# Performance work log

Measured on AMD Instinct MI355X. Metric: run time of the kernel, lower is better.

## Reference

```python
import jax, jax.numpy as jnp
import numpy as np

B, L, D = 4, 1024, 256
H, HD, W = 8, 64, 3


def setup_inputs() -> dict:
    key = jax.random.key(0)
    ks = jax.random.split(key, 5)
    return {
        'x': jax.random.normal(ks[0], (B, L, D), dtype=jnp.float32),
        'Wq': jax.random.normal(ks[1], (D, H * HD), dtype=jnp.float32) * 0.05,
        'bq': jnp.zeros((H, 1, 1, HD), dtype=jnp.float32),
        'Wk': jax.random.normal(ks[2], (D, H * HD), dtype=jnp.float32) * 0.05,
        'bk': jnp.zeros((H, 1, 1, HD), dtype=jnp.float32),
        'Wv': jax.random.normal(ks[3], (D, H), dtype=jnp.float32) * 0.05,
        'pe': jax.random.normal(ks[4], (L, D), dtype=jnp.float32) * 0.05,
    }


def reference(x, Wq, bq, Wk, bk, Wv, pe):
    b, l, d = x.shape
    h, hd = bq.shape[0], bq.shape[-1]
    xpe = x + pe  # learned positional encoding added for Q and K only
    # tf.split over axis 3 into h heads + concat axis 0 == reshape then head-major transpose
    q = (xpe @ Wq).reshape(b, l, h, hd).transpose(2, 0, 1, 3) + bq  # [H,B,L,hd]
    k = (xpe @ Wk).reshape(b, l, h, hd).transpose(2, 0, 1, 3) + bk  # [H,B,L,hd]
    v = jax.nn.sigmoid(x @ Wv).transpose(2, 0, 1)  # [H,B,L]
    att = jnp.einsum('hbqd,hbkd->hbqk', q, k) / jnp.sqrt(jnp.asarray(hd, x.dtype))
    att = jax.nn.softmax(att, axis=-1)  # [H,B,L,L]
    # band_part(0,-1) + diag_part(k=(0,L-1)) + transpose + reverse(-2,-1) is
    # equivalent to: out[.., jp, dist] = att[.., n-dist, n] with n = L-1-jp, masked n-dist>=0
    jp = jnp.arange(l)
    n = l - 1 - jp                      # reversed position index, [L]
    m = n[:, None] - jp[None, :]        # row (query) index per (pos, distance), [L,L]
    valid = m >= 0
    g = att[:, :, jnp.clip(m, 0), n[:, None]]  # gather diagonals -> [H,B,L,L]
    a = jnp.where(valid, g, jnp.asarray(0, x.dtype)) * v[:, :, :, None]
    # avg pool over the distance (last) axis, window W, stride 1, SAME,
    # TF AvgPool excludes padding from the count
    ssum = jax.lax.reduce_window(a, 0.0, jax.lax.add, (1, 1, 1, W), (1, 1, 1, 1), 'SAME')
    cnt = jax.lax.reduce_window(jnp.ones((l,), a.dtype), 0.0, jax.lax.add, (W,), (1,), 'SAME')
    a = ssum / cnt  # [H,B,L,L]
    # global_mode: permute to [B, pos, dist, H] and sum over positions
    return a.transpose(1, 2, 3, 0).sum(axis=1)  # [B, L, H]
```

## Files before the change

### kernel.cpp

```cpp
#include <hip/hip_runtime.h>
#include <hip/hip_bf16.h>
#include <math.h>

#define B 4
#define L 1024
#define D 256
#define H 8
#define HD 64

#define KB_OFF  1048576
#define VR_OFF  2097152
#define TP2_OFF (VR_OFF + 32768)
#define T_OFF   (TP2_OFF + 2097152)
#define XP_OFF  (T_OFF + 32768)
#define WT_OFF  (XP_OFF + 524288)

typedef short short8 __attribute__((ext_vector_type(8)));
typedef float f32x16 __attribute__((ext_vector_type(16)));

__device__ __forceinline__ unsigned short f2bf(float f) {
  __hip_bfloat16 h = __float2bfloat16(f);
  return *reinterpret_cast<unsigned short*>(&h);
}

__global__ __launch_bounds__(256) void prep_wx_kernel(
    const float* __restrict__ x, const float* __restrict__ Wq,
    const float* __restrict__ Wk, const float* __restrict__ Wv,
    const float* __restrict__ pe, float* __restrict__ ws)
{
  const int tid = threadIdx.x;
  if (blockIdx.x < 32) {
    __shared__ float lds[32][257];
    const int c0 = blockIdx.x * 32;
    const float* W = (c0 < 512) ? Wq : Wk;
    const int cc = c0 & 511;
    const int c = tid & 31, dd = tid >> 5;
    for (int d0 = 0; d0 < 256; d0 += 8)
      lds[c][d0 + dd] = W[(d0 + dd) * 512 + cc + c];
    __syncthreads();
    __hip_bfloat16* WT = (__hip_bfloat16*)(ws + WT_OFF);
    for (int cl = 0; cl < 32; ++cl)
      WT[(c0 + cl) * 256 + tid] = __float2bfloat16(lds[cl][tid]);
    return;
  }

  __shared__ float xs[8][257];
  const int r0 = (blockIdx.x - 32) * 8;
  __hip_bfloat16* XP = (__hip_bfloat16*)(ws + XP_OFF);
  for (int idx = tid; idx < 2048; idx += 256) {
    int rr = idx >> 8, c = idx & 255;
    int gr = r0 + rr, l = gr & 1023;
    float xv = x[gr * 256 + c];
    xs[rr][c] = xv;
    XP[gr * 256 + c] = __float2bfloat16(xv + pe[l * 256 + c]);
  }
  __syncthreads();
  {
    int rr = tid >> 5, h = (tid >> 2) & 7, t4 = tid & 3;
    float acc = 0.f;
    const int d0 = t4 << 6;
#pragma unroll 16
    for (int d = 0; d < 64; ++d) acc += xs[rr][d0 + d] * Wv[(d0 + d) * 8 + h];
    acc += __shfl_down(acc, 1, 4);
    acc += __shfl_down(acc, 2, 4);
    if (t4 == 0) {
      float v = 1.f / (1.f + __expf(-acc));
      int gr = r0 + rr;
      int b = gr >> 10, l = gr & 1023;
      ws[VR_OFF + (h * 4 + b) * 1024 + (1023 - l)] = v;
    }
  }
}

__global__ __launch_bounds__(256) void qkgemm_kernel(float* __restrict__ ws,
    const float* __restrict__ bq, const float* __restrict__ bk)
{
  const int tid = threadIdx.x;
  const int w = tid >> 6, lane = tid & 63;
  const int wid = blockIdx.x * 4 + w;
  const int lt = wid & 127;
  const int cp = wid >> 7;

  const __hip_bfloat16* XP = (const __hip_bfloat16*)(ws + XP_OFF);
  const __hip_bfloat16* WT = (const __hip_bfloat16*)(ws + WT_OFF);

  const int ln = (lt << 5) + (lane & 31);
  const int dlo = (lane >> 5) << 3;
  const int ca = (cp << 6) + (lane & 31);
  const __hip_bfloat16* xr = XP + ln * 256 + dlo;
  const __hip_bfloat16* ar = WT + ca * 256 + dlo;
  const __hip_bfloat16* br = ar + (32 * 256);

  f32x16 acca = {0.f,0.f,0.f,0.f,0.f,0.f,0.f,0.f,0.f,0.f,0.f,0.f,0.f,0.f,0.f,0.f};
  f32x16 accb = {0.f,0.f,0.f,0.f,0.f,0.f,0.f,0.f,0.f,0.f,0.f,0.f,0.f,0.f,0.f,0.f};
#pragma unroll
  for (int k = 0; k < 16; ++k) {
    short8 bf  = *(const short8*)(xr + k * 16);
    short8 afa = *(const short8*)(ar + k * 16);
    short8 afb = *(const short8*)(br + k * 16);
    acca = __builtin_amdgcn_mfma_f32_32x32x16_bf16(afa, bf, acca, 0, 0, 0);
    accb = __builtin_amdgcn_mfma_f32_32x32x16_bf16(afb, bf, accb, 0, 0, 0);
  }

  const int b = ln >> 10, l = ln & 1023;
  const int hq = cp & 7;
  const int hi4 = (lane >> 5) << 2;
  const float* bias = (cp < 8) ? bq : bk;
  const int cbase = hq << 6;
  __hip_bfloat16* base = (__hip_bfloat16*)ws + ((cp < 8) ? 0 : (size_t)KB_OFF * 2);
  __hip_bfloat16* dst = base + ((((size_t)(hq * 4 + b) << 10) + l) << 6);

#pragma unroll
  for (int q = 0; q < 4; ++q) {
    int hd0 = (q << 3) + hi4;
    float4 bv = *(const float4*)(bias + cbase + hd0);
    ushort4 pk;
    pk.x = f2bf(acca[4 * q + 0] + bv.x);
    pk.y = f2bf(acca[4 * q + 1] + bv.y);
    pk.z = f2bf(acca[4 * q + 2] + bv.z);
    pk.w = f2bf(acca[4 * q + 3] + bv.w);
    *(ushort4*)(dst + hd0) = pk;

    int hd1 = hd0 + 32;
    float4 bw = *(const float4*)(bias + cbase + hd1);
    ushort4 pk2;
    pk2.x = f2bf(accb[4 * q + 0] + bw.x);
    pk2.y = f2bf(accb[4 * q + 1] + bw.y);
    pk2.z = f2bf(accb[4 * q + 2] + bw.z);
    pk2.w = f2bf(accb[4 * q + 3] + bw.w);
    *(ushort4*)(dst + hd1) = pk2;
  }
}

__global__ __launch_bounds__(256) void attn_kernel(float* __restrict__ ws)
{
  __shared__ __hip_bfloat16 Ks[256 * 64];
  __shared__ float smerge[4][32];
  const int tid = threadIdx.x;
  const int w = tid >> 6, lane = tid & 63;
  const int i = blockIdx.x;
  const int hb = i & 31;
  const int j = i >> 5;
  const int qt = (j & 8) ? ((j < 16) ? 23 - j : 55 - j) : j;

  const __hip_bfloat16* Qb = (const __hip_bfloat16*)ws + ((size_t)hb << 16);
  const __hip_bfloat16* Kb = (const __hip_bfloat16*)(ws + KB_OFF) + ((size_t)hb << 16);
  const float* __restrict__ vr = ws + VR_OFF + (hb << 10);

  const int qrow = (qt << 5) + (lane & 31);
  const int dlo = (lane >> 5) << 3;
  const int coff = (lane >> 5) << 2;

  const __hip_bfloat16* qr = Qb + (qrow << 6) + dlo;
  short8 qf0 = *(const short8*)(qr);
  short8 qf1 = *(const short8*)(qr + 16);
  short8 qf2 = *(const short8*)(qr + 32);
  short8 qf3 = *(const short8*)(qr + 48);

#define STAGE8(c)                                                             \
  {                                                                           \
    const float4* src_ = (const float4*)Kb + ((c) << 11);                     \
    _Pragma("unroll")                                                         \
    for (int u = 0; u < 8; ++u) {                                             \
      int idx_ = (u << 8) + tid;                                              \
      float4 v_ = src_[idx_];                                                 \
      int row_ = idx_ >> 3;                                                   \
      int colb_ = (idx_ & 7) << 4;                                            \
      *(float4*)((char*)Ks + row_ * 128 + (colb_ ^ ((row_ & 7) << 4))) = v_;  \
    }                                                                         \
  }

#define LDK(tl, kf)                                                           \
  {                                                                           \
    int row_ = ((tl) << 5) + (lane & 31);                                     \
    int sw_ = (row_ & 7) << 4;                                                \
    int cb_ = (lane >> 5) << 4;                                               \
    char* bp_ = (char*)Ks + row_ * 128;                                       \
    kf[0] = *(const short8*)(bp_ + ((cb_) ^ sw_));                            \
    kf[1] = *(const short8*)(bp_ + ((cb_ + 32) ^ sw_));                       \
    kf[2] = *(const short8*)(bp_ + ((cb_ + 64) ^ sw_));                       \
    kf[3] = *(const short8*)(bp_ + ((cb_ + 96) ^ sw_));                       \
  }

  float sp0 = 0.f, sp1 = 0.f, sp2 = 0.f, sp3 = 0.f;
  for (int c = 0; c < 4; ++c) {
    if (c) __syncthreads();
    STAGE8(c);
    __syncthreads();
    short8 ka[4], kb[4];
    LDK(w, ka);
    LDK(w + 4, kb);
    f32x16 acca = {0.f,0.f,0.f,0.f,0.f,0.f,0.f,0.f,0.f,0.f,0.f,0.f,0.f,0.f,0.f,0.f};
    f32x16 accb = {0.f,0.f,0.f,0.f,0.f,0.f,0.f,0.f,0.f,0.f,0.f,0.f,0.f,0.f,0.f,0.f};
    acca = __builtin_amdgcn_mfma_f32_32x32x16_bf16(ka[0], qf0, acca, 0, 0, 0);
    accb = __builtin_amdgcn_mfma_f32_32x32x16_bf16(kb[0], qf0, accb, 0, 0, 0);
    acca = __builtin_amdgcn_mfma_f32_32x32x16_bf16(ka[1], qf1, acca, 0, 0, 0);
    accb = __builtin_amdgcn_mfma_f32_32x32x16_bf16(kb[1], qf1, accb, 0, 0, 0);
    acca = __builtin_amdgcn_mfma_f32_32x32x16_bf16(ka[2], qf2, acca, 0, 0, 0);
    accb = __builtin_amdgcn_mfma_f32_32x32x16_bf16(kb[2], qf2, accb, 0, 0, 0);
    acca = __builtin_amdgcn_mfma_f32_32x32x16_bf16(ka[3], qf3, acca, 0, 0, 0);
    accb = __builtin_amdgcn_mfma_f32_32x32x16_bf16(kb[3], qf3, accb, 0, 0, 0);
#pragma unroll
    for (int r = 0; r < 16; r += 2) {
      sp0 += __expf(acca[r] * 0.125f);
      sp1 += __expf(acca[r + 1] * 0.125f);
      sp2 += __expf(accb[r] * 0.125f);
      sp3 += __expf(accb[r + 1] * 0.125f);
    }
  }
  float s_part = (sp0 + sp1) + (sp2 + sp3);
  s_part += __shfl_xor(s_part, 32);
  if (lane < 32) smerge[w][lane] = s_part;
  __syncthreads();
  const int q = lane & 31;
  const float inv = 1.f / (smerge[0][q] + smerge[1][q] + smerge[2][q] + smerge[3][q]);

#define FLUSH(dt_, acc_)                                                      \
  {                                                                           \
    const int kt_ = qt + (dt_);                                               \
    const float* vb_ = vr + (kt_ << 5) + coff;                                \
    float4 v0_ = *(const float4*)(vb_);                                       \
    float4 v1_ = *(const float4*)(vb_ + 8);                                   \
    float4 v2_ = *(const float4*)(vb_ + 16);                                  \
    float4 v3_ = *(const float4*)(vb_ + 24);                                  \
    float p_[16];                                                             \
    _Pragma("unroll")                                                         \
    for (int r = 0; r < 16; ++r) {                                            \
      float vv_ = (r < 4) ? (&v0_.x)[r] : (r < 8) ? (&v1_.x)[r - 4]           \
                : (r < 12) ? (&v2_.x)[r - 8] : (&v3_.x)[r - 12];              \
      p_[r] = __expf(acc_[r] * 0.125f) * vv_ * inv;                           \
    }                                                                         \
    float accg_ = 0.f;                                                        \
    _Pragma("unroll")                                                         \
    for (int hi = 0; hi < 2; ++hi)                                            \
      _Pragma("unroll")                                                       \
      for (int r = 0; r < 16; ++r) {                                          \
        const int km_ = (hi << 2) + (r & 3) + ((r >> 2) << 3);                \
        int src_ = ((hi << 5) + km_ + 31 - lane) & 63;                        \
        float g_ = __shfl(p_[r], src_);                                       \
        if (km_ <= lane && km_ >= lane - 31) accg_ += g_;                     \
      }                                                                       \
    ws[TP2_OFF + ((size_t)hb << 16) + ((((qt) << 5) + (dt_)) << 6) + lane] = accg_; \
  }

  const int c0 = qt >> 3;
  for (int c = 3; c >= c0; --c) {
    if (c != 3) {
      __syncthreads();
      STAGE8(c);
      __syncthreads();
    }
    const int kta = (c << 3) + w;
    const int ktb = kta + 4;
    if (kta >= qt) {
      short8 ka[4], kb[4];
      LDK(w, ka);
      LDK(w + 4, kb);
      f32x16 acca = {0.f,0.f,0.f,0.f,0.f,0.f,0.f,0.f,0.f,0.f,0.f,0.f,0.f,0.f,0.f,0.f};
      f32x16 accb = {0.f,0.f,0.f,0.f,0.f,0.f,0.f,0.f,0.f,0.f,0.f,0.f,0.f,0.f,0.f,0.f};
      acca = __builtin_amdgcn_mfma_f32_32x32x16_bf16(ka[0], qf0, acca, 0, 0, 0);
      accb = __builtin_amdgcn_mfma_f32_32x32x16_bf16(kb[0], qf0, accb, 0, 0, 0);
      acca = __builtin_amdgcn_mfma_f32_32x32x16_bf16(ka[1], qf1, acca, 0, 0, 0);
      accb = __builtin_amdgcn_mfma_f32_32x32x16_bf16(kb[1], qf1, accb, 0, 0, 0);
      acca = __builtin_amdgcn_mfma_f32_32x32x16_bf16(ka[2], qf2, acca, 0, 0, 0);
      accb = __builtin_amdgcn_mfma_f32_32x32x16_bf16(kb[2], qf2, accb, 0, 0, 0);
      acca = __builtin_amdgcn_mfma_f32_32x32x16_bf16(ka[3], qf3, acca, 0, 0, 0);
      accb = __builtin_amdgcn_mfma_f32_32x32x16_bf16(kb[3], qf3, accb, 0, 0, 0);
      FLUSH(kta - qt, acca);
      FLUSH(ktb - qt, accb);
    } else if (ktb >= qt) {
      short8 kb[4];
      LDK(w + 4, kb);
      f32x16 accb = {0.f,0.f,0.f,0.f,0.f,0.f,0.f,0.f,0.f,0.f,0.f,0.f,0.f,0.f,0.f,0.f};
      accb = __builtin_amdgcn_mfma_f32_32x32x16_bf16(kb[0], qf0, accb, 0, 0, 0);
      accb = __builtin_amdgcn_mfma_f32_32x32x16_bf16(kb[1], qf1, accb, 0, 0, 0);
      accb = __builtin_amdgcn_mfma_f32_32x32x16_bf16(kb[2], qf2, accb, 0, 0, 0);
      accb = __builtin_amdgcn_mfma_f32_32x32x16_bf16(kb[3], qf3, accb, 0, 0, 0);
      FLUSH(ktb - qt, accb);
    }
  }
}

__global__ __launch_bounds__(256) void out1_kernel(float* __restrict__ ws)
{
  const int tid = threadIdx.x;
  const int i = blockIdx.x;
  const int hb = i & 31;
  const int jc = i >> 5;
  const int jj = (jc << 5) + (tid >> 3);
  const int t8 = tid & 7;
  const float* TP = ws + TP2_OFF + ((size_t)hb << 16);

  float acc = 0.f;
  const int s = jj + 31;
#pragma unroll
  for (int cand = 0; cand < 2; ++cand) {
    int dt = (s >> 5) - cand;
    if (dt < 0 || dt > 31) continue;
    int idx = s - (dt << 5);
    int qmax = 31 - dt;
    for (int qt = t8; qt <= qmax; qt += 8)
      acc += TP[(((qt << 5) + dt) << 6) + idx];
  }
  acc += __shfl_down(acc, 4, 8);
  acc += __shfl_down(acc, 2, 8);
  acc += __shfl_down(acc, 1, 8);
  if (t8 == 0) ws[T_OFF + (hb << 10) + jj] = acc;
}

__global__ __launch_bounds__(256) void out2_kernel(const float* __restrict__ ws,
                                                   float* __restrict__ out)
{
  __shared__ float s[130];
  const int tid = threadIdx.x;
  const int i = blockIdx.x;
  const int hb = i & 31;
  const int jc = i >> 5;
  const int j0 = jc << 7;
  const float* T = ws + T_OFF + (hb << 10);

  if (tid < 130) {
    int j = j0 + tid - 1;
    s[tid] = (j >= 0 && j < 1024) ? T[j] : 0.f;
  }
  __syncthreads();
  if (tid < 128) {
    int j = j0 + tid;
    float cnt = (j == 0 || j == 1023) ? 2.f : 3.f;
    float v = (s[tid] + s[tid + 1] + s[tid + 2]) / cnt;
    int h = hb >> 2, b = hb & 3;
    out[(((b << 10) + j) << 3) + h] = v;
  }
}

extern "C" void kernel_launch(void* const* d_in, const int* in_sizes, int n_in,
                              void* d_out, int out_size, void* d_ws, size_t ws_size,
                              hipStream_t stream)
{
  const float* x  = (const float*)d_in[0];
  const float* Wq = (const float*)d_in[1];
  const float* bq = (const float*)d_in[2];
  const float* Wk = (const float*)d_in[3];
  const float* bk = (const float*)d_in[4];
  const float* Wv = (const float*)d_in[5];
  const float* pe = (const float*)d_in[6];
  float* ws = (float*)d_ws;
  float* out = (float*)d_out;

  prep_wx_kernel<<<dim3(544), dim3(256), 0, stream>>>(x, Wq, Wk, Wv, pe, ws);
  qkgemm_kernel<<<dim3(512), dim3(256), 0, stream>>>(ws, bq, bk);
  attn_kernel<<<dim3(1024), dim3(256), 0, stream>>>(ws);
  out1_kernel<<<dim3(1024), dim3(256), 0, stream>>>(ws);
  out2_kernel<<<dim3(256), dim3(256), 0, stream>>>(ws, out);
}
```

Measured before the change: 61.44 us.

## Fuse output reduction and pooling kernels, vectorize prep loads, split GEMM accumulators

Merges the diagonal-sum kernel and the avg-pool kernel into one launch that recomputes the two halo sums per block in shared memory. This removes a launch and the intermediate T buffer. The prep kernel now loads x and pe as float4 and stores packed bf16 quads. The QK GEMM splits the k-loop into two independent accumulator chains per output to shorten the MFMA dependency chain, at the cost of more registers and a final add.

```diff
diff --git a/kernel.cpp b/kernel.cpp
--- a/kernel.cpp
+++ b/kernel.cpp
@@ -11,8 +11,7 @@
 #define KB_OFF  1048576
 #define VR_OFF  2097152
 #define TP2_OFF (VR_OFF + 32768)
-#define T_OFF   (TP2_OFF + 2097152)
-#define XP_OFF  (T_OFF + 32768)
+#define XP_OFF  (TP2_OFF + 2097152)
 #define WT_OFF  (XP_OFF + 524288)
 
 typedef short short8 __attribute__((ext_vector_type(8)));
@@ -47,12 +46,20 @@
   __shared__ float xs[8][257];
   const int r0 = (blockIdx.x - 32) * 8;
   __hip_bfloat16* XP = (__hip_bfloat16*)(ws + XP_OFF);
-  for (int idx = tid; idx < 2048; idx += 256) {
-    int rr = idx >> 8, c = idx & 255;
-    int gr = r0 + rr, l = gr & 1023;
-    float xv = x[gr * 256 + c];
-    xs[rr][c] = xv;
-    XP[gr * 256 + c] = __float2bfloat16(xv + pe[l * 256 + c]);
+#pragma unroll
+  for (int u = 0; u < 2; ++u) {
+    int idx = (u << 8) + tid;
+    int row = idx >> 6, c4 = idx & 63;
+    int gr = r0 + row, l = gr & 1023;
+    float4 xv = ((const float4*)(x + (size_t)gr * 256))[c4];
+    float4 pv = ((const float4*)(pe + (size_t)l * 256))[c4];
+    int c = c4 << 2;
+    xs[row][c] = xv.x; xs[row][c + 1] = xv.y;
+    xs[row][c + 2] = xv.z; xs[row][c + 3] = xv.w;
+    ushort4 pk;
+    pk.x = f2bf(xv.x + pv.x); pk.y = f2bf(xv.y + pv.y);
+    pk.z = f2bf(xv.z + pv.z); pk.w = f2bf(xv.w + pv.w);
+    *(ushort4*)(XP + (size_t)gr * 256 + c) = pk;
   }
   __syncthreads();
   {
@@ -91,16 +98,26 @@
   const __hip_bfloat16* ar = WT + ca * 256 + dlo;
   const __hip_bfloat16* br = ar + (32 * 256);
 
-  f32x16 acca = {0.f,0.f,0.f,0.f,0.f,0.f,0.f,0.f,0.f,0.f,0.f,0.f,0.f,0.f,0.f,0.f};
-  f32x16 accb = {0.f,0.f,0.f,0.f,0.f,0.f,0.f,0.f,0.f,0.f,0.f,0.f,0.f,0.f,0.f,0.f};
-#pragma unroll
-  for (int k = 0; k < 16; ++k) {
-    short8 bf  = *(const short8*)(xr + k * 16);
-    short8 afa = *(const short8*)(ar + k * 16);
-    short8 afb = *(const short8*)(br + k * 16);
-    acca = __builtin_amdgcn_mfma_f32_32x32x16_bf16(afa, bf, acca, 0, 0, 0);
-    accb = __builtin_amdgcn_mfma_f32_32x32x16_bf16(afb, bf, accb, 0, 0, 0);
-  }
+  f32x16 a0 = {0.f,0.f,0.f,0.f,0.f,0.f,0.f,0.f,0.f,0.f,0.f,0.f,0.f,0.f,0.f,0.f};
+  f32x16 a1 = {0.f,0.f,0.f,0.f,0.f,0.f,0.f,0.f,0.f,0.f,0.f,0.f,0.f,0.f,0.f,0.f};
+  f32x16 b0 = {0.f,0.f,0.f,0.f,0.f,0.f,0.f,0.f,0.f,0.f,0.f,0.f,0.f,0.f,0.f,0.f};
+  f32x16 b1 = {0.f,0.f,0.f,0.f,0.f,0.f,0.f,0.f,0.f,0.f,0.f,0.f,0.f,0.f,0.f,0.f};
+#pragma unroll
+  for (int k = 0; k < 8; ++k) {
+    short8 bfA = *(const short8*)(xr + k * 16);
+    short8 bfB = *(const short8*)(xr + (k + 8) * 16);
+    short8 afa0 = *(const short8*)(ar + k * 16);
+    short8 afa1 = *(const short8*)(ar + (k + 8) * 16);
+    short8 afb0 = *(const short8*)(br + k * 16);
+    short8 afb1 = *(const short8*)(br + (k + 8) * 16);
+    a0 = __builtin_amdgcn_mfma_f32_32x32x16_bf16(afa0, bfA, a0, 0, 0, 0);
+    a1 = __builtin_amdgcn_mfma_f32_32x32x16_bf16(afa1, bfB, a1, 0, 0, 0);
+    b0 = __builtin_amdgcn_mfma_f32_32x32x16_bf16(afb0, bfA, b0, 0, 0, 0);
+    b1 = __builtin_amdgcn_mfma_f32_32x32x16_bf16(afb1, bfB, b1, 0, 0, 0);
+  }
+  f32x16 acca, accb;
+#pragma unroll
+  for (int r = 0; r < 16; ++r) { acca[r] = a0[r] + a1[r]; accb[r] = b0[r] + b1[r]; }
 
   const int b = ln >> 10, l = ln & 1023;
   const int hq = cp & 7;
@@ -281,53 +298,55 @@
   }
 }
 
-__global__ __launch_bounds__(256) void out1_kernel(float* __restrict__ ws)
-{
+__global__ __launch_bounds__(256) void out_kernel(const float* __restrict__ ws,
+                                                  float* __restrict__ out)
+{
+  __shared__ float sT[34];
   const int tid = threadIdx.x;
   const int i = blockIdx.x;
   const int hb = i & 31;
   const int jc = i >> 5;
-  const int jj = (jc << 5) + (tid >> 3);
-  const int t8 = tid & 7;
+  const int j0 = jc << 5;
   const float* TP = ws + TP2_OFF + ((size_t)hb << 16);
 
-  float acc = 0.f;
-  const int s = jj + 31;
-#pragma unroll
-  for (int cand = 0; cand < 2; ++cand) {
-    int dt = (s >> 5) - cand;
-    if (dt < 0 || dt > 31) continue;
-    int idx = s - (dt << 5);
-    int qmax = 31 - dt;
-    for (int qt = t8; qt <= qmax; qt += 8)
-      acc += TP[(((qt << 5) + dt) << 6) + idx];
-  }
-  acc += __shfl_down(acc, 4, 8);
-  acc += __shfl_down(acc, 2, 8);
-  acc += __shfl_down(acc, 1, 8);
-  if (t8 == 0) ws[T_OFF + (hb << 10) + jj] = acc;
-}
-
-__global__ __launch_bounds__(256) void out2_kernel(const float* __restrict__ ws,
-                                                   float* __restrict__ out)
-{
-  __shared__ float s[130];
-  const int tid = threadIdx.x;
-  const int i = blockIdx.x;
-  const int hb = i & 31;
-  const int jc = i >> 5;
-  const int j0 = jc << 7;
-  const float* T = ws + T_OFF + (hb << 10);
-
-  if (tid < 130) {
-    int j = j0 + tid - 1;
-    s[tid] = (j >= 0 && j < 1024) ? T[j] : 0.f;
+#define TSUM(jj_, t8_, res_)                                                  \
+  {                                                                           \
+    float acc_ = 0.f;                                                         \
+    if ((jj_) >= 0 && (jj_) < 1024) {                                         \
+      const int s_ = (jj_) + 31;                                              \
+      _Pragma("unroll")                                                       \
+      for (int cand = 0; cand < 2; ++cand) {                                  \
+        int dt = (s_ >> 5) - cand;                                            \
+        if (dt < 0 || dt > 31) continue;                                      \
+        int idx = s_ - (dt << 5);                                             \
+        int qmax = 31 - dt;                                                   \
+        for (int qt = (t8_); qt <= qmax; qt += 8)                             \
+          acc_ += TP[(((qt << 5) + dt) << 6) + idx];                          \
+      }                                                                       \
+    }                                                                         \
+    acc_ += __shfl_down(acc_, 4, 8);                                          \
+    acc_ += __shfl_down(acc_, 2, 8);                                          \
+    acc_ += __shfl_down(acc_, 1, 8);                                          \
+    res_ = acc_;                                                              \
+  }
+
+  {
+    int jloc = tid >> 3, t8 = tid & 7;
+    float r;
+    TSUM(j0 + jloc - 1, t8, r);
+    if (t8 == 0) sT[jloc] = r;
+  }
+  if (tid < 16) {
+    int jx = tid >> 3, t8 = tid & 7;
+    float r;
+    TSUM(j0 + 31 + jx, t8, r);
+    if (t8 == 0) sT[32 + jx] = r;
   }
   __syncthreads();
-  if (tid < 128) {
+  if (tid < 32) {
     int j = j0 + tid;
     float cnt = (j == 0 || j == 1023) ? 2.f : 3.f;
-    float v = (s[tid] + s[tid + 1] + s[tid + 2]) / cnt;
+    float v = (sT[tid] + sT[tid + 1] + sT[tid + 2]) / cnt;
     int h = hb >> 2, b = hb & 3;
     out[(((b << 10) + j) << 3) + h] = v;
   }
@@ -350,6 +369,5 @@
   prep_wx_kernel<<<dim3(544), dim3(256), 0, stream>>>(x, Wq, Wk, Wv, pe, ws);
   qkgemm_kernel<<<dim3(512), dim3(256), 0, stream>>>(ws, bq, bk);
   attn_kernel<<<dim3(1024), dim3(256), 0, stream>>>(ws);
-  out1_kernel<<<dim3(1024), dim3(256), 0, stream>>>(ws);
-  out2_kernel<<<dim3(256), dim3(256), 0, stream>>>(ws, out);
-}
+  out_kernel<<<dim3(1024), dim3(256), 0, stream>>>(ws, out);
+}
```

Result: faster. 59.27 us (median of 2 runs) (-3.5%).
